# Optimization experiments

Measured on AMD Instinct MI355X. Metric: run time of the kernel, lower is better.

The kernel has to match this reference:

```python
import jax, jax.numpy as jnp
import numpy as np

EMBED = 1024
HEADS = 16


def setup_inputs() -> dict:
    key = jax.random.key(0)
    ks = jax.random.split(key, 7)
    scale = 1.0 / np.sqrt(EMBED)
    x = jax.random.normal(ks[0], (4, 2048, EMBED), dtype=jnp.float32)
    Wq = jax.random.normal(ks[1], (EMBED, EMBED), dtype=jnp.float32) * scale
    bq = jax.random.normal(ks[2], (EMBED,), dtype=jnp.float32) * 0.01
    Wk = jax.random.normal(ks[3], (EMBED, EMBED), dtype=jnp.float32) * scale
    bk = jax.random.normal(ks[4], (EMBED,), dtype=jnp.float32) * 0.01
    Wv = jax.random.normal(ks[5], (EMBED, EMBED), dtype=jnp.float32) * scale
    bv = jax.random.normal(ks[6], (EMBED,), dtype=jnp.float32) * 0.01
    return {"x": x, "Wq": Wq, "bq": bq, "Wk": Wk, "bk": bk, "Wv": Wv, "bv": bv}


def reference(x, Wq, bq, Wk, bk, Wv, bv):
    b, s, n = x.shape
    h = HEADS
    d = n // h
    # torch nn.Linear: y = x @ W.T + b
    q = (jnp.einsum("bsn,mn->bsm", x, Wq) + bq).reshape(b, s, h, d).transpose(0, 2, 1, 3)
    k = (jnp.einsum("bsn,mn->bsm", x, Wk) + bk).reshape(b, s, h, d).transpose(0, 2, 1, 3)
    v = (jnp.einsum("bsn,mn->bsm", x, Wv) + bv).reshape(b, s, h, d).transpose(0, 2, 1, 3)
    # scores: [b, h, s_q, s_k]; fixed scale of 1/10 as in the source
    scores = jnp.einsum("bhqd,bhkd->bhqk", q, k) / 10.0
    # NOTE: softmax over dim=-2 (the QUERY axis), matching the source exactly
    attn = jax.nn.softmax(scores, axis=-2)
    out = jnp.einsum("bhqk,bhkd->bhqd", attn, v)
    return out.transpose(0, 2, 1, 3).reshape(b, s, n)
```

## Files before the change

### kernel.cpp

```cpp
#include <hip/hip_runtime.h>
#include <math.h>

#define SEQ    2048
#define EMBED  1024
#define HEADS  16
#define HDIM   64
#define BATCH  4
#define ROWS   (BATCH * SEQ)
#define BH     (BATCH * HEADS)

typedef _Float16 f16;
typedef __attribute__((ext_vector_type(8))) _Float16 f16x8;
typedef __attribute__((ext_vector_type(4))) _Float16 f16x4;
typedef __attribute__((ext_vector_type(4))) float    f32x4;

#define LOG2E_10 0.14426950408889634f

__device__ __forceinline__ float fast_exp2(float x) { return __builtin_amdgcn_exp2f(x); }
__device__ __forceinline__ float fast_log2(float x) { return __builtin_amdgcn_logf(x); }

__device__ __forceinline__ void async16(void* l, const void* g) {
    __builtin_amdgcn_global_load_lds(
        (__attribute__((address_space(1))) void*)(uintptr_t)g,
        (__attribute__((address_space(3))) void*)(uint32_t)(uintptr_t)l,
        16, 0, 0);
}
__device__ __forceinline__ void async4(void* l, const void* g) {
    __builtin_amdgcn_global_load_lds(
        (__attribute__((address_space(1))) void*)(uintptr_t)g,
        (__attribute__((address_space(3))) void*)(uint32_t)(uintptr_t)l,
        4, 0, 0);
}

__device__ __forceinline__ f32x4 mfma16(f16x8 a, f16x8 b, f32x4 c) {
    return __builtin_amdgcn_mfma_f32_16x16x32_f16(a, b, c, 0, 0, 0);
}
__device__ __forceinline__ f32x4 mfma16k16(f16x4 a, f16x4 b, f32x4 c) {
    return __builtin_amdgcn_mfma_f32_16x16x16f16(a, b, c, 0, 0, 0);
}

#define NX4 (ROWS * EMBED / 4)
#define NW4 (EMBED * EMBED / 4)
__global__ __launch_bounds__(256) void cvt_kernel(
    const float* __restrict__ x,
    const float* __restrict__ Wq, const float* __restrict__ Wk,
    const float* __restrict__ Wv,
    f16* __restrict__ xh, f16* __restrict__ Wh)
{
    int i = blockIdx.x * 256 + threadIdx.x;
    const float4* src; f16* dst; int j;
    if (i < NX4)              { src = (const float4*)x;  dst = xh;                j = i; }
    else if (i < NX4 + NW4)   { src = (const float4*)Wq; dst = Wh;                j = i - NX4; }
    else if (i < NX4 + 2*NW4) { src = (const float4*)Wk; dst = Wh + EMBED*EMBED;  j = i - NX4 - NW4; }
    else                      { src = (const float4*)Wv; dst = Wh + 2*EMBED*EMBED;j = i - NX4 - 2*NW4; }
    float4 v = src[j];
    f16x4 h;
    h[0] = (f16)v.x; h[1] = (f16)v.y; h[2] = (f16)v.z; h[3] = (f16)v.w;
    *(f16x4*)(dst + (size_t)j * 4) = h;
}

__global__ __launch_bounds__(256) void proj_kernel(
    const f16* __restrict__ A,
    const f16* __restrict__ W,
    const float* __restrict__ bq, const float* __restrict__ bk,
    const float* __restrict__ bv,
    f16* __restrict__ Qh, f16* __restrict__ Kh, f16* __restrict__ Vt)
{
    __shared__ f16 As[128 * 32];
    __shared__ f16 Bs[128 * 32];

    const int t = threadIdx.x, wv = t >> 6, lane = t & 63;
    const int lm = lane & 15, quad = lane >> 4;
    const int r0 = blockIdx.x * 128, c0 = blockIdx.y * 128;
    const int wm = wv & 1, wn = wv >> 1;

    const int srow = wv * 32 + (lane >> 2);
    const int sch  = (lane & 3) * 8;
    const f16* gA = A + (size_t)(r0 + srow) * EMBED + sch;
    const f16* gB = W + (size_t)(c0 + srow) * EMBED + sch;
    f16* lA = As + wv * 1024;
    f16* lB = Bs + wv * 1024;

    f32x4 acc[4][4];
#pragma unroll
    for (int i = 0; i < 4; ++i)
#pragma unroll
        for (int j = 0; j < 4; ++j) acc[i][j] = (f32x4){0.f, 0.f, 0.f, 0.f};

    for (int kk = 0; kk < EMBED; kk += 32) {
        __syncthreads();
        async16(lA,        gA + kk);
        async16(lA + 512,  gA + 16 * EMBED + kk);
        async16(lB,        gB + kk);
        async16(lB + 512,  gB + 16 * EMBED + kk);
        __syncthreads();

        f16x8 af[4], bf[4];
#pragma unroll
        for (int i = 0; i < 4; ++i)
            af[i] = *(const f16x8*)&As[(wm * 64 + i * 16 + lm) * 32 + quad * 8];
#pragma unroll
        for (int i = 0; i < 4; ++i)
            bf[i] = *(const f16x8*)&Bs[(wn * 64 + i * 16 + lm) * 32 + quad * 8];
#pragma unroll
        for (int mi = 0; mi < 4; ++mi)
#pragma unroll
            for (int ni = 0; ni < 4; ++ni)
                acc[mi][ni] = mfma16(af[mi], bf[ni], acc[mi][ni]);
    }

    const int z = c0 >> 10;
    const float* bias = (z == 0) ? bq : (z == 1) ? bk : bv;
#pragma unroll
    for (int ni = 0; ni < 4; ++ni) {
        int col = c0 + wn * 64 + ni * 16 + lm;
        int cz  = col & 1023;
        float bb = bias[cz];
        int h = cz >> 6, d = cz & 63;
#pragma unroll
        for (int mi = 0; mi < 4; ++mi) {
            int rbase = r0 + wm * 64 + mi * 16 + quad * 4;
            int b = rbase >> 11, s = rbase & 2047;
            if (z < 2) {
                f16* O = (z == 0) ? Qh : Kh;
                size_t base = ((size_t)(b * HEADS + h) * SEQ + s) * HDIM + d;
#pragma unroll
                for (int r = 0; r < 4; ++r)
                    O[base + (size_t)r * HDIM] = (f16)(acc[mi][ni][r] + bb);
            } else {
                f16x4 pk;
#pragma unroll
                for (int r = 0; r < 4; ++r) pk[r] = (f16)(acc[mi][ni][r] + bb);
                *(f16x4*)&Vt[((size_t)(b * HEADS + h) * HDIM + d) * SEQ + s] = pk;
            }
        }
    }
}

__device__ __forceinline__ void xcd_decode(int d, int& bh, int& x128) {
    int xcd  = d & 7;
    int r    = d >> 3;
    x128     = (r & 15) * 128;
    bh       = (r >> 4) * 8 + xcd;
}

__global__ __launch_bounds__(256) void stats_kernel(
    const f16* __restrict__ Qh, const f16* __restrict__ Kh,
    float* __restrict__ lgv)
{
    __shared__ f16 Ks[128 * 64];
    __shared__ f16 Qs[64 * 64];

    const int t = threadIdx.x, wv = t >> 6, lane = t & 63;
    const int lm = lane & 15, quad = lane >> 4;
    int bh, k0;
    xcd_decode(blockIdx.x, bh, k0);
    const int grow = lane >> 3;
    const int gsw  = ((lane & 7) ^ grow) * 8;
    const int rs   = lm & 7;
    const size_t base = (size_t)bh * SEQ * HDIM;

#pragma unroll
    for (int i = 0; i < 4; ++i) {
        int g = wv * 4 + i;
        async16(Ks + g * 512, Kh + base + (size_t)(k0 + g * 8 + grow) * HDIM + gsw);
    }
    __syncthreads();

    f16x8 kf[2][2];
#pragma unroll
    for (int ct = 0; ct < 2; ++ct)
#pragma unroll
        for (int ds = 0; ds < 2; ++ds)
            kf[ct][ds] = *(const f16x8*)&Ks[(wv * 32 + ct * 16 + lm) * 64
                                            + (((ds * 4 + quad) ^ rs) << 3)];

    float cs0 = 0.f, cs1 = 0.f;
    for (int q0 = 0; q0 < SEQ; q0 += 64) {
        __syncthreads();
#pragma unroll
        for (int i = 0; i < 2; ++i) {
            int g = wv * 2 + i;
            async16(Qs + g * 512, Qh + base + (size_t)(q0 + g * 8 + grow) * HDIM + gsw);
        }
        __syncthreads();
#pragma unroll
        for (int qt = 0; qt < 4; ++qt) {
            f16x8 a0 = *(const f16x8*)&Qs[(qt * 16 + lm) * 64 + ((quad ^ rs) << 3)];
            f16x8 a1 = *(const f16x8*)&Qs[(qt * 16 + lm) * 64 + (((4 + quad) ^ rs) << 3)];
            f32x4 c0v = (f32x4){0.f, 0.f, 0.f, 0.f};
            f32x4 c1v = (f32x4){0.f, 0.f, 0.f, 0.f};
            c0v = mfma16(a0, kf[0][0], c0v); c0v = mfma16(a1, kf[0][1], c0v);
            c1v = mfma16(a0, kf[1][0], c1v); c1v = mfma16(a1, kf[1][1], c1v);
#pragma unroll
            for (int r = 0; r < 4; ++r) {
                cs0 += fast_exp2(c0v[r] * LOG2E_10);
                cs1 += fast_exp2(c1v[r] * LOG2E_10);
            }
        }
    }
    cs0 += __shfl_xor(cs0, 16, 64); cs0 += __shfl_xor(cs0, 32, 64);
    cs1 += __shfl_xor(cs1, 16, 64); cs1 += __shfl_xor(cs1, 32, 64);
    if (quad == 0) {
        lgv[(size_t)bh * SEQ + k0 + wv * 32 + lm]      = 10.0f - fast_log2(cs0);
        lgv[(size_t)bh * SEQ + k0 + wv * 32 + 16 + lm] = 10.0f - fast_log2(cs1);
    }
}

__global__ __launch_bounds__(256) void out_kernel(
    const f16* __restrict__ Qh, const f16* __restrict__ Kh,
    const f16* __restrict__ Vt, const float* __restrict__ lgv,
    float* __restrict__ out)
{
    __shared__ f16 L[24576 + 512];

    const int t = threadIdx.x, wv = t >> 6, lane = t & 63;
    const int lm = lane & 15, quad = lane >> 4;
    const int wq = wv >> 1, wk = wv & 1;
    int bh, q0;
    xcd_decode(blockIdx.x, bh, q0);
    const int b = bh >> 4, h = bh & 15;
    const int grow = lane >> 3;
    const int gsw  = ((lane & 7) ^ grow) * 8;
    const int rs   = lm & 7;
    const size_t base = (size_t)bh * SEQ * HDIM;

    f16* Qs = L;

#pragma unroll
    for (int i = 0; i < 4; ++i) {
        int g = wv * 4 + i;
        async16(Qs + g * 512, Qh + base + (size_t)(q0 + g * 8 + grow) * HDIM + gsw);
    }
#pragma unroll
    for (int i = 0; i < 2; ++i) {
        int g = wv * 2 + i;
        async16(L + 8192  + g * 512, Kh + base + (size_t)(g * 8 + grow) * HDIM + gsw);
        async16(L + 16384 + g * 512, Vt + base + (size_t)(g * 8 + grow) * SEQ + gsw);
    }
    if (wv == 0) async4((float*)(L + 24576), lgv + (size_t)bh * SEQ + lane);
    __syncthreads();

    f16x8 qa[4][2];
#pragma unroll
    for (int qt = 0; qt < 4; ++qt)
#pragma unroll
        for (int ds = 0; ds < 2; ++ds)
            qa[qt][ds] = *(const f16x8*)&Qs[(wq * 64 + qt * 16 + lm) * 64
                                            + (((ds * 4 + quad) ^ rs) << 3)];

    f32x4 oacc[4][4];
#pragma unroll
    for (int i = 0; i < 4; ++i)
#pragma unroll
        for (int j = 0; j < 4; ++j) oacc[i][j] = (f32x4){0.f, 0.f, 0.f, 0.f};

    for (int it = 0; it < SEQ / 64; ++it) {
        const int cur = it & 1;
        if (it + 1 < SEQ / 64) {
            const int nxt = cur ^ 1, k0n = (it + 1) * 64;
            f16* Kb = L + 8192  + nxt * 4096;
            f16* Vb = L + 16384 + nxt * 4096;
#pragma unroll
            for (int i = 0; i < 2; ++i) {
                int g = wv * 2 + i;
                async16(Kb + g * 512, Kh + base + (size_t)(k0n + g * 8 + grow) * HDIM + gsw);
                async16(Vb + g * 512, Vt + base + (size_t)(g * 8 + grow) * SEQ + k0n + gsw);
            }
            if (wv == 0) async4((float*)(L + 24576) + nxt * 64,
                                lgv + (size_t)bh * SEQ + k0n + lane);
        }
        const f16* Kb = L + 8192  + cur * 4096;
        const f16* Vb = L + 16384 + cur * 4096;
        const float* Lb = (const float*)(L + 24576) + cur * 64;

#pragma unroll
        for (int ct = 0; ct < 2; ++ct) {
            const int kb = wk * 32 + ct * 16;
            f16x8 kf0 = *(const f16x8*)&Kb[(kb + lm) * 64 + ((quad ^ rs) << 3)];
            f16x8 kf1 = *(const f16x8*)&Kb[(kb + lm) * 64 + (((4 + quad) ^ rs) << 3)];
            f32x4 lg4 = *(const f32x4*)&Lb[kb + quad * 4];
            const int vch = ((wk * 4 + ct * 2 + (quad >> 1)) ^ rs);
            f16x4 vb[4];
#pragma unroll
            for (int dt = 0; dt < 4; ++dt)
                vb[dt] = *(const f16x4*)&Vb[(dt * 16 + lm) * 64 + vch * 8 + (quad & 1) * 4];
#pragma unroll
            for (int qt = 0; qt < 4; ++qt) {
                f32x4 s4 = (f32x4){0.f, 0.f, 0.f, 0.f};
                s4 = mfma16(kf0, qa[qt][0], s4);
                s4 = mfma16(kf1, qa[qt][1], s4);
                f16x4 pa;
#pragma unroll
                for (int r = 0; r < 4; ++r)
                    pa[r] = (f16)fast_exp2(s4[r] * LOG2E_10 + lg4[r]);
#pragma unroll
                for (int dt = 0; dt < 4; ++dt)
                    oacc[qt][dt] = mfma16k16(pa, vb[dt], oacc[qt][dt]);
            }
        }
        __syncthreads();
    }

    float* red = (float*)L;
    if (wk == 1) {
#pragma unroll
        for (int qt = 0; qt < 4; ++qt)
#pragma unroll
            for (int dt = 0; dt < 4; ++dt)
#pragma unroll
                for (int r = 0; r < 4; ++r)
                    red[wq * 4096 + (qt * 16 + quad * 4 + r) * 64 + dt * 16 + lm]
                        = oacc[qt][dt][r];
    }
    __syncthreads();
    if (wk == 0) {
        const float inv1024 = 1.0f / 1024.0f;
#pragma unroll
        for (int qt = 0; qt < 4; ++qt)
#pragma unroll
            for (int dt = 0; dt < 4; ++dt) {
                int col = h * HDIM + dt * 16 + lm;
#pragma unroll
                for (int r = 0; r < 4; ++r) {
                    int ql = qt * 16 + quad * 4 + r;
                    int s  = q0 + wq * 64 + ql;
                    float v = oacc[qt][dt][r]
                            + red[wq * 4096 + ql * 64 + dt * 16 + lm];
                    out[((size_t)b * SEQ + s) * EMBED + col] = v * inv1024;
                }
            }
    }
}

extern "C" void kernel_launch(void* const* d_in, const int* in_sizes, int n_in,
                              void* d_out, int out_size, void* d_ws, size_t ws_size,
                              hipStream_t stream) {
    const float* x  = (const float*)d_in[0];
    const float* Wq = (const float*)d_in[1];
    const float* bq = (const float*)d_in[2];
    const float* Wk = (const float*)d_in[3];
    const float* bk = (const float*)d_in[4];
    const float* Wv = (const float*)d_in[5];
    const float* bv = (const float*)d_in[6];
    float* out = (float*)d_out;

    f16* xh = (f16*)d_ws;
    f16* Wh = xh + (size_t)ROWS * EMBED;
    f16* Qh = Wh + (size_t)3 * EMBED * EMBED;
    f16* Kh = Qh + (size_t)BH * SEQ * HDIM;
    f16* Vt = Kh + (size_t)BH * SEQ * HDIM;
    float* lgv = (float*)(Vt + (size_t)BH * SEQ * HDIM);

    cvt_kernel<<<(NX4 + 3 * NW4) / 256, 256, 0, stream>>>(x, Wq, Wk, Wv, xh, Wh);
    proj_kernel<<<dim3(ROWS / 128, 3 * EMBED / 128), 256, 0, stream>>>(
        xh, Wh, bq, bk, bv, Qh, Kh, Vt);
    stats_kernel<<<dim3(SEQ / 128 * BH), 256, 0, stream>>>(Qh, Kh, lgv);
    out_kernel<<<dim3(SEQ / 128 * BH), 256, 0, stream>>>(Qh, Kh, Vt, lgv, out);
}
```

Before: 300.8 us.

## Fold softmax scale into Q and column normalizer into pre-scaled V

Multiplies Q by log2(e)/10 in the projection epilogue, so the score exponent needs no scaling multiply. The stats kernel now also rescales each V column by 1024/colsum and writes a normalized V copy into the freed xh buffer. The out kernel then just exponentiates scores and multiplies by the prescaled V, which drops the per-column log-stat loads and the add from the inner loop. Q fragments are loaded directly from global memory instead of through LDS, which reduces shared memory use. The costs are an extra V read and write pass in the stats kernel, and possible fp16 range or precision loss: exp2 is no longer offset by the stat, and the 1024 factor must stay in range.

After: 323.0 us. +7.4%, slower.

```diff
diff --git a/kernel.cpp b/kernel.cpp
--- a/kernel.cpp
+++ b/kernel.cpp
@@ -17,19 +17,12 @@
 #define LOG2E_10 0.14426950408889634f
 
 __device__ __forceinline__ float fast_exp2(float x) { return __builtin_amdgcn_exp2f(x); }
-__device__ __forceinline__ float fast_log2(float x) { return __builtin_amdgcn_logf(x); }
 
 __device__ __forceinline__ void async16(void* l, const void* g) {
     __builtin_amdgcn_global_load_lds(
         (__attribute__((address_space(1))) void*)(uintptr_t)g,
         (__attribute__((address_space(3))) void*)(uint32_t)(uintptr_t)l,
         16, 0, 0);
-}
-__device__ __forceinline__ void async4(void* l, const void* g) {
-    __builtin_amdgcn_global_load_lds(
-        (__attribute__((address_space(1))) void*)(uintptr_t)g,
-        (__attribute__((address_space(3))) void*)(uint32_t)(uintptr_t)l,
-        4, 0, 0);
 }
 
 __device__ __forceinline__ f32x4 mfma16(f16x8 a, f16x8 b, f32x4 c) {
@@ -111,6 +104,7 @@
 
     const int z = c0 >> 10;
     const float* bias = (z == 0) ? bq : (z == 1) ? bk : bv;
+    const float osc = (z == 0) ? LOG2E_10 : 1.0f;
 #pragma unroll
     for (int ni = 0; ni < 4; ++ni) {
         int col = c0 + wn * 64 + ni * 16 + lm;
@@ -126,7 +120,7 @@
                 size_t base = ((size_t)(b * HEADS + h) * SEQ + s) * HDIM + d;
 #pragma unroll
                 for (int r = 0; r < 4; ++r)
-                    O[base + (size_t)r * HDIM] = (f16)(acc[mi][ni][r] + bb);
+                    O[base + (size_t)r * HDIM] = (f16)((acc[mi][ni][r] + bb) * osc);
             } else {
                 f16x4 pk;
 #pragma unroll
@@ -146,7 +140,7 @@
 
 __global__ __launch_bounds__(256) void stats_kernel(
     const f16* __restrict__ Qh, const f16* __restrict__ Kh,
-    float* __restrict__ lgv)
+    const f16* __restrict__ Vt, f16* __restrict__ Vt2)
 {
     __shared__ f16 Ks[128 * 64];
     __shared__ f16 Qs[64 * 64];
@@ -194,25 +188,40 @@
             c1v = mfma16(a0, kf[1][0], c1v); c1v = mfma16(a1, kf[1][1], c1v);
 #pragma unroll
             for (int r = 0; r < 4; ++r) {
-                cs0 += fast_exp2(c0v[r] * LOG2E_10);
-                cs1 += fast_exp2(c1v[r] * LOG2E_10);
+                cs0 += fast_exp2(c0v[r]);
+                cs1 += fast_exp2(c1v[r]);
             }
         }
     }
     cs0 += __shfl_xor(cs0, 16, 64); cs0 += __shfl_xor(cs0, 32, 64);
     cs1 += __shfl_xor(cs1, 16, 64); cs1 += __shfl_xor(cs1, 32, 64);
+
+    __syncthreads();
+    float* sc = (float*)Qs;
     if (quad == 0) {
-        lgv[(size_t)bh * SEQ + k0 + wv * 32 + lm]      = 10.0f - fast_log2(cs0);
-        lgv[(size_t)bh * SEQ + k0 + wv * 32 + 16 + lm] = 10.0f - fast_log2(cs1);
+        sc[wv * 32 + lm]      = 1024.0f / cs0;
+        sc[wv * 32 + 16 + lm] = 1024.0f / cs1;
+    }
+    __syncthreads();
+    const int row = t >> 2, cb = (t & 3) * 32;
+    const f16* src = Vt  + base + (size_t)row * SEQ + k0 + cb;
+    f16*       dst = Vt2 + base + (size_t)row * SEQ + k0 + cb;
+#pragma unroll
+    for (int c = 0; c < 4; ++c) {
+        f16x8 v = *(const f16x8*)(src + c * 8);
+        f16x8 o;
+#pragma unroll
+        for (int j = 0; j < 8; ++j)
+            o[j] = (f16)((float)v[j] * sc[cb + c * 8 + j]);
+        *(f16x8*)(dst + c * 8) = o;
     }
 }
 
 __global__ __launch_bounds__(256) void out_kernel(
     const f16* __restrict__ Qh, const f16* __restrict__ Kh,
-    const f16* __restrict__ Vt, const float* __restrict__ lgv,
-    float* __restrict__ out)
+    const f16* __restrict__ Vt2, float* __restrict__ out)
 {
-    __shared__ f16 L[24576 + 512];
+    __shared__ f16 L[16384];
 
     const int t = threadIdx.x, wv = t >> 6, lane = t & 63;
     const int lm = lane & 15, quad = lane >> 4;
@@ -225,29 +234,25 @@
     const int rs   = lm & 7;
     const size_t base = (size_t)bh * SEQ * HDIM;
 
-    f16* Qs = L;
-
-#pragma unroll
-    for (int i = 0; i < 4; ++i) {
-        int g = wv * 4 + i;
-        async16(Qs + g * 512, Qh + base + (size_t)(q0 + g * 8 + grow) * HDIM + gsw);
-    }
+    f16* Ks = L;
+    f16* Vs = L + 8192;
+
+    f16x8 qa[4][2];
+#pragma unroll
+    for (int qt = 0; qt < 4; ++qt)
+#pragma unroll
+        for (int ds = 0; ds < 2; ++ds)
+            qa[qt][ds] = *(const f16x8*)(Qh + base
+                          + (size_t)(q0 + wq * 64 + qt * 16 + lm) * HDIM
+                          + ds * 32 + quad * 8);
+
 #pragma unroll
     for (int i = 0; i < 2; ++i) {
         int g = wv * 2 + i;
-        async16(L + 8192  + g * 512, Kh + base + (size_t)(g * 8 + grow) * HDIM + gsw);
-        async16(L + 16384 + g * 512, Vt + base + (size_t)(g * 8 + grow) * SEQ + gsw);
-    }
-    if (wv == 0) async4((float*)(L + 24576), lgv + (size_t)bh * SEQ + lane);
-    __syncthreads();
-
-    f16x8 qa[4][2];
-#pragma unroll
-    for (int qt = 0; qt < 4; ++qt)
-#pragma unroll
-        for (int ds = 0; ds < 2; ++ds)
-            qa[qt][ds] = *(const f16x8*)&Qs[(wq * 64 + qt * 16 + lm) * 64
-                                            + (((ds * 4 + quad) ^ rs) << 3)];
+        async16(Ks + g * 512, Kh  + base + (size_t)(g * 8 + grow) * HDIM + gsw);
+        async16(Vs + g * 512, Vt2 + base + (size_t)(g * 8 + grow) * SEQ + gsw);
+    }
+    __syncthreads();
 
     f32x4 oacc[4][4];
 #pragma unroll
@@ -259,27 +264,23 @@
         const int cur = it & 1;
         if (it + 1 < SEQ / 64) {
             const int nxt = cur ^ 1, k0n = (it + 1) * 64;
-            f16* Kb = L + 8192  + nxt * 4096;
-            f16* Vb = L + 16384 + nxt * 4096;
 #pragma unroll
             for (int i = 0; i < 2; ++i) {
                 int g = wv * 2 + i;
-                async16(Kb + g * 512, Kh + base + (size_t)(k0n + g * 8 + grow) * HDIM + gsw);
-                async16(Vb + g * 512, Vt + base + (size_t)(g * 8 + grow) * SEQ + k0n + gsw);
-            }
-            if (wv == 0) async4((float*)(L + 24576) + nxt * 64,
-                                lgv + (size_t)bh * SEQ + k0n + lane);
-        }
-        const f16* Kb = L + 8192  + cur * 4096;
-        const f16* Vb = L + 16384 + cur * 4096;
-        const float* Lb = (const float*)(L + 24576) + cur * 64;
+                async16(Ks + nxt * 4096 + g * 512,
+                        Kh + base + (size_t)(k0n + g * 8 + grow) * HDIM + gsw);
+                async16(Vs + nxt * 4096 + g * 512,
+                        Vt2 + base + (size_t)(g * 8 + grow) * SEQ + k0n + gsw);
+            }
+        }
+        const f16* Kb = Ks + cur * 4096;
+        const f16* Vb = Vs + cur * 4096;
 
 #pragma unroll
         for (int ct = 0; ct < 2; ++ct) {
             const int kb = wk * 32 + ct * 16;
             f16x8 kf0 = *(const f16x8*)&Kb[(kb + lm) * 64 + ((quad ^ rs) << 3)];
             f16x8 kf1 = *(const f16x8*)&Kb[(kb + lm) * 64 + (((4 + quad) ^ rs) << 3)];
-            f32x4 lg4 = *(const f32x4*)&Lb[kb + quad * 4];
             const int vch = ((wk * 4 + ct * 2 + (quad >> 1)) ^ rs);
             f16x4 vb[4];
 #pragma unroll
@@ -293,7 +294,7 @@
                 f16x4 pa;
 #pragma unroll
                 for (int r = 0; r < 4; ++r)
-                    pa[r] = (f16)fast_exp2(s4[r] * LOG2E_10 + lg4[r]);
+                    pa[r] = (f16)fast_exp2(s4[r]);
 #pragma unroll
                 for (int dt = 0; dt < 4; ++dt)
                     oacc[qt][dt] = mfma16k16(pa, vb[dt], oacc[qt][dt]);
@@ -350,11 +351,11 @@
     f16* Qh = Wh + (size_t)3 * EMBED * EMBED;
     f16* Kh = Qh + (size_t)BH * SEQ * HDIM;
     f16* Vt = Kh + (size_t)BH * SEQ * HDIM;
-    float* lgv = (float*)(Vt + (size_t)BH * SEQ * HDIM);
+    f16* Vt2 = xh;
 
     cvt_kernel<<<(NX4 + 3 * NW4) / 256, 256, 0, stream>>>(x, Wq, Wk, Wv, xh, Wh);
     proj_kernel<<<dim3(ROWS / 128, 3 * EMBED / 128), 256, 0, stream>>>(
         xh, Wh, bq, bk, bv, Qh, Kh, Vt);
-    stats_kernel<<<dim3(SEQ / 128 * BH), 256, 0, stream>>>(Qh, Kh, lgv);
-    out_kernel<<<dim3(SEQ / 128 * BH), 256, 0, stream>>>(Qh, Kh, Vt, lgv, out);
-}
+    stats_kernel<<<dim3(SEQ / 128 * BH), 256, 0, stream>>>(Qh, Kh, Vt, Vt2);
+    out_kernel<<<dim3(SEQ / 128 * BH), 256, 0, stream>>>(Qh, Kh, Vt2, out);
+}
```
